# Kernel tuning notes

Hardware: AMD Instinct MI355X
Metric: run time of the kernel (lower is better)

## Reference

```python
import jax, jax.numpy as jnp
import numpy as np

REG1 = 0.5
REG2 = 0.5
ALPHA = 0.5

def setup_inputs() -> dict:
    key = jax.random.key(0)
    k1, k2, k3, k4, k5 = jax.random.split(key, 5)
    N, D, K = 32768, 256, 2048
    return {
        "encoder_out": jax.random.normal(k1, (N, D), dtype=jnp.float32),
        "prototypes": jax.random.normal(k2, (K, D), dtype=jnp.float32),
        "recon_loss": jax.random.uniform(k3, (), dtype=jnp.float32),
        "kl_loss": jax.random.uniform(k4, (), dtype=jnp.float32),
        "mmd_loss": jax.random.uniform(k5, (), dtype=jnp.float32),
    }


def _cdist_min_loss(z, prototypes):
    # torch.cdist(z, protos) -> [N, K]; f_dist = cdist(protos, z) = its transpose.
    # prototypes accessed via .data in torch -> detached.
    p = jax.lax.stop_gradient(prototypes)
    z2 = jnp.sum(z * z, axis=1, keepdims=True)          # [N, 1]
    p2 = jnp.sum(p * p, axis=1)                          # [K]
    sq = z2 + p2[None, :] - 2.0 * (z @ p.T)              # [N, K]
    dist = jnp.sqrt(jnp.maximum(sq, 0.0))
    p_min = jnp.min(dist, axis=1).mean()   # p_dist.min(1).values.mean()
    f_min = jnp.min(dist, axis=0).mean()   # f_dist [K,N].min(1) == dist.min(0)
    return REG1 * p_min + REG2 * f_min


def reference(encoder_out, prototypes, recon_loss, kl_loss, mmd_loss):
    cvae_loss = recon_loss + ALPHA * kl_loss + mmd_loss
    prot_decoding_loss = _cdist_min_loss(encoder_out, prototypes)
    # no projection head (use_projector=False)
    x = encoder_out / jnp.maximum(
        jnp.linalg.norm(encoder_out, axis=1, keepdims=True), 1e-12)
    x_mapped = x @ prototypes.T  # [N, K]
    return (encoder_out, x, x_mapped, cvae_loss, prot_decoding_loss)
```

## Files before the change

kernel.cpp:

```cpp
#include <hip/hip_runtime.h>
#include <hip/hip_bf16.h>

typedef __bf16 bf16x8 __attribute__((ext_vector_type(8)));
typedef float  f32x4  __attribute__((ext_vector_type(4)));

#define N_ROWS 32768
#define D_DIM  256
#define K_PROT 2048

#define WS_Z2    0
#define WS_INVN  32768
#define WS_P2    65536
#define WS_RMIN  67584
#define WS_CMIN  100352

#define OUT_X0   0UL
#define OUT_X1   8388608UL
#define OUT_XMAP 16777216UL
#define OUT_CVAE 83886080UL
#define OUT_PROT 83886081UL

__global__ __launch_bounds__(256) void k1_rows(
    const float* __restrict__ Z, float* __restrict__ out0, float* __restrict__ out1,
    float* __restrict__ z2, float* __restrict__ invn, unsigned int* __restrict__ rmin)
{
    int row  = (blockIdx.x << 2) + (threadIdx.x >> 6);
    int lane = threadIdx.x & 63;
    size_t base = (size_t)row * D_DIM;
    float4 v = ((const float4*)(Z + base))[lane];
    float ss = v.x*v.x + v.y*v.y + v.z*v.z + v.w*v.w;
    #pragma unroll
    for (int d = 32; d >= 1; d >>= 1) ss += __shfl_xor(ss, d);
    float inv = 1.0f / fmaxf(sqrtf(ss), 1e-12f);
    ((float4*)(out0 + base))[lane] = v;
    float4 xv; xv.x = v.x*inv; xv.y = v.y*inv; xv.z = v.z*inv; xv.w = v.w*inv;
    ((float4*)(out1 + base))[lane] = xv;
    if (lane == 0) { z2[row] = ss; invn[row] = inv; rmin[row] = 0x7f800000u; }
}

__global__ __launch_bounds__(256) void k2_prot(
    const float* __restrict__ P, float* __restrict__ p2, unsigned int* __restrict__ cmin)
{
    int row  = (blockIdx.x << 2) + (threadIdx.x >> 6);
    int lane = threadIdx.x & 63;
    float4 v = ((const float4*)(P + (size_t)row * D_DIM))[lane];
    float ss = v.x*v.x + v.y*v.y + v.z*v.z + v.w*v.w;
    #pragma unroll
    for (int d = 32; d >= 1; d >>= 1) ss += __shfl_xor(ss, d);
    if (lane == 0) { p2[row] = ss; cmin[row] = 0x7f800000u; }
}

#define BM 128
#define BN 128
#define LDSS 40

__global__ __launch_bounds__(256, 2) void k3_gemm(
    const float* __restrict__ Z, const float* __restrict__ P,
    const float* __restrict__ z2, const float* __restrict__ p2,
    const float* __restrict__ invn,
    float* __restrict__ xmap,
    unsigned int* __restrict__ rmin, unsigned int* __restrict__ cmin)
{
    __shared__ __bf16 As[BM * LDSS];
    __shared__ __bf16 Bs[BN * LDSS];

    const int tid  = threadIdx.x;
    const int bn   = blockIdx.x & 15;
    const int bm   = blockIdx.x >> 4;
    const int lane = tid & 63;
    const int wave = tid >> 6;
    const int wm   = wave >> 1;
    const int wn   = wave & 1;
    const int l15  = lane & 15;
    const int quad = lane >> 4;

    const int m0 = bm * BM;
    const int n0 = bn * BN;

    const int srow = tid >> 1;
    const int scol = (tid & 1) << 4;

    f32x4 acc[4][4];
    #pragma unroll
    for (int i = 0; i < 4; i++)
        #pragma unroll
        for (int j = 0; j < 4; j++)
            #pragma unroll
            for (int r = 0; r < 4; r++) acc[i][j][r] = 0.0f;

    for (int kt = 0; kt < D_DIM; kt += 32) {
        const float* aSrc = Z + (size_t)(m0 + srow) * D_DIM + kt + scol;
        const float* bSrc = P + (size_t)(n0 + srow) * D_DIM + kt + scol;
        float4 a0 = ((const float4*)aSrc)[0];
        float4 a1 = ((const float4*)aSrc)[1];
        float4 a2 = ((const float4*)aSrc)[2];
        float4 a3 = ((const float4*)aSrc)[3];
        float4 b0 = ((const float4*)bSrc)[0];
        float4 b1 = ((const float4*)bSrc)[1];
        float4 b2 = ((const float4*)bSrc)[2];
        float4 b3 = ((const float4*)bSrc)[3];

        __syncthreads();

        __bf16* aDst = As + srow * LDSS + scol;
        __bf16* bDst = Bs + srow * LDSS + scol;
        {
            bf16x8 w;
            w[0]=(__bf16)a0.x; w[1]=(__bf16)a0.y; w[2]=(__bf16)a0.z; w[3]=(__bf16)a0.w;
            w[4]=(__bf16)a1.x; w[5]=(__bf16)a1.y; w[6]=(__bf16)a1.z; w[7]=(__bf16)a1.w;
            *(bf16x8*)aDst = w;
            w[0]=(__bf16)a2.x; w[1]=(__bf16)a2.y; w[2]=(__bf16)a2.z; w[3]=(__bf16)a2.w;
            w[4]=(__bf16)a3.x; w[5]=(__bf16)a3.y; w[6]=(__bf16)a3.z; w[7]=(__bf16)a3.w;
            *(bf16x8*)(aDst + 8) = w;
            w[0]=(__bf16)b0.x; w[1]=(__bf16)b0.y; w[2]=(__bf16)b0.z; w[3]=(__bf16)b0.w;
            w[4]=(__bf16)b1.x; w[5]=(__bf16)b1.y; w[6]=(__bf16)b1.z; w[7]=(__bf16)b1.w;
            *(bf16x8*)bDst = w;
            w[0]=(__bf16)b2.x; w[1]=(__bf16)b2.y; w[2]=(__bf16)b2.z; w[3]=(__bf16)b2.w;
            w[4]=(__bf16)b3.x; w[5]=(__bf16)b3.y; w[6]=(__bf16)b3.z; w[7]=(__bf16)b3.w;
            *(bf16x8*)(bDst + 8) = w;
        }
        __syncthreads();

        bf16x8 af[4], bf[4];
        #pragma unroll
        for (int i = 0; i < 4; i++)
            af[i] = *(const bf16x8*)(As + (wm*64 + i*16 + l15) * LDSS + quad*8);
        #pragma unroll
        for (int j = 0; j < 4; j++)
            bf[j] = *(const bf16x8*)(Bs + (wn*64 + j*16 + l15) * LDSS + quad*8);
        #pragma unroll
        for (int i = 0; i < 4; i++)
            #pragma unroll
            for (int j = 0; j < 4; j++)
                acc[i][j] = __builtin_amdgcn_mfma_f32_16x16x32_bf16(af[i], bf[j], acc[i][j], 0, 0, 0);
    }

    float invr[16], zzr[16];
    #pragma unroll
    for (int i = 0; i < 4; i++)
        #pragma unroll
        for (int r = 0; r < 4; r++) {
            int gm = m0 + wm*64 + i*16 + quad*4 + r;
            invr[i*4+r] = invn[gm];
            zzr[i*4+r]  = z2[gm];
        }
    float pp[4];
    #pragma unroll
    for (int j = 0; j < 4; j++) pp[j] = p2[n0 + wn*64 + j*16 + l15];

    float cminv[4] = {3.0e38f, 3.0e38f, 3.0e38f, 3.0e38f};

    #pragma unroll
    for (int i = 0; i < 4; i++) {
        #pragma unroll
        for (int r = 0; r < 4; r++) {
            int gm = m0 + wm*64 + i*16 + quad*4 + r;
            float zi = zzr[i*4+r], iv = invr[i*4+r];
            size_t orow = (size_t)gm * K_PROT + n0 + wn*64 + l15;
            float rv = 3.0e38f;
            #pragma unroll
            for (int j = 0; j < 4; j++) {
                float g = acc[i][j][r];
                xmap[orow + j*16] = g * iv;
                float d = sqrtf(fmaxf(zi + pp[j] - 2.0f*g, 0.0f));
                rv = fminf(rv, d);
                cminv[j] = fminf(cminv[j], d);
            }
            #pragma unroll
            for (int s = 1; s < 16; s <<= 1) rv = fminf(rv, __shfl_xor(rv, s));
            if (l15 == 0) atomicMin(&rmin[gm], __float_as_uint(rv));
        }
    }
    #pragma unroll
    for (int j = 0; j < 4; j++) {
        float cv = cminv[j];
        cv = fminf(cv, __shfl_xor(cv, 16));
        cv = fminf(cv, __shfl_xor(cv, 32));
        if (quad == 0) atomicMin(&cmin[n0 + wn*64 + j*16 + l15], __float_as_uint(cv));
    }
}

__global__ __launch_bounds__(1024) void k4_final(
    const float* __restrict__ rminf, const float* __restrict__ cminf,
    const float* __restrict__ recon, const float* __restrict__ kl,
    const float* __restrict__ mmd, float* __restrict__ out)
{
    __shared__ float sr[16], sc[16];
    int tid = threadIdx.x;
    float a = 0.0f, b = 0.0f;
    for (int i = tid; i < N_ROWS; i += 1024) a += rminf[i];
    for (int i = tid; i < K_PROT; i += 1024) b += cminf[i];
    #pragma unroll
    for (int d = 32; d >= 1; d >>= 1) { a += __shfl_xor(a, d); b += __shfl_xor(b, d); }
    int w = tid >> 6, lane = tid & 63;
    if (lane == 0) { sr[w] = a; sc[w] = b; }
    __syncthreads();
    if (tid == 0) {
        float SA = 0.0f, SB = 0.0f;
        #pragma unroll
        for (int i = 0; i < 16; i++) { SA += sr[i]; SB += sc[i]; }
        out[OUT_CVAE] = recon[0] + 0.5f*kl[0] + mmd[0];
        out[OUT_PROT] = 0.5f*(SA / (float)N_ROWS) + 0.5f*(SB / (float)K_PROT);
    }
}

extern "C" void kernel_launch(void* const* d_in, const int* in_sizes, int n_in,
                              void* d_out, int out_size, void* d_ws, size_t ws_size,
                              hipStream_t stream)
{
    const float* Z     = (const float*)d_in[0];
    const float* P     = (const float*)d_in[1];
    const float* recon = (const float*)d_in[2];
    const float* kl    = (const float*)d_in[3];
    const float* mmd   = (const float*)d_in[4];
    float* out = (float*)d_out;
    float* ws  = (float*)d_ws;

    float* z2   = ws + WS_Z2;
    float* invn = ws + WS_INVN;
    float* p2   = ws + WS_P2;
    unsigned int* rmin = (unsigned int*)(ws + WS_RMIN);
    unsigned int* cmin = (unsigned int*)(ws + WS_CMIN);

    hipLaunchKernelGGL(k1_rows, dim3(N_ROWS/4), dim3(256), 0, stream,
                       Z, out + OUT_X0, out + OUT_X1, z2, invn, rmin);
    hipLaunchKernelGGL(k2_prot, dim3(K_PROT/4), dim3(256), 0, stream, P, p2, cmin);
    hipLaunchKernelGGL(k3_gemm, dim3((N_ROWS/BM)*(K_PROT/BN)), dim3(256), 0, stream,
                       Z, P, z2, p2, invn, out + OUT_XMAP, rmin, cmin);
    hipLaunchKernelGGL(k4_final, dim3(1), dim3(1024), 0, stream,
                       (const float*)rmin, (const float*)cmin, recon, kl, mmd, out);
}
```

Measured before the change: 443.9 us.

## Pre-convert inputs to bf16 and stage GEMM tiles via direct global-to-LDS loads

The row-norm kernels now also write bf16 copies of the encoder output and prototypes into workspace. The GEMM reads these with global_load_lds 16-byte direct-to-LDS transfers instead of loading fp32, converting in registers and storing to LDS. BK grows from 32 to 64, which halves the number of K iterations and barriers. The intent is to cut the GEMM's global traffic and VALU conversion work per tile. In exchange the unpadded LDS layout may cause bank conflicts on fragment reads, and the extra bf16 writes add traffic in the prep kernels.

```diff
diff --git a/kernel.cpp b/kernel.cpp
--- a/kernel.cpp
+++ b/kernel.cpp
@@ -2,6 +2,7 @@
 #include <hip/hip_bf16.h>
 
 typedef __bf16 bf16x8 __attribute__((ext_vector_type(8)));
+typedef __bf16 bf16x4 __attribute__((ext_vector_type(4)));
 typedef float  f32x4  __attribute__((ext_vector_type(4)));
 
 #define N_ROWS 32768
@@ -13,6 +14,8 @@
 #define WS_P2    65536
 #define WS_RMIN  67584
 #define WS_CMIN  100352
+#define WS_ZB    102400
+#define WS_PB    (102400 + 4194304)
 
 #define OUT_X0   0UL
 #define OUT_X1   8388608UL
@@ -20,9 +23,16 @@
 #define OUT_CVAE 83886080UL
 #define OUT_PROT 83886081UL
 
+__device__ __forceinline__ void gload16(const __bf16* gsrc, const __bf16* ldst) {
+    auto g = (const __attribute__((address_space(1))) unsigned int*)(unsigned long long)gsrc;
+    auto l = (__attribute__((address_space(3))) unsigned int*)(unsigned long long)ldst;
+    __builtin_amdgcn_global_load_lds(g, l, 16, 0, 0);
+}
+
 __global__ __launch_bounds__(256) void k1_rows(
     const float* __restrict__ Z, float* __restrict__ out0, float* __restrict__ out1,
-    float* __restrict__ z2, float* __restrict__ invn, unsigned int* __restrict__ rmin)
+    float* __restrict__ z2, float* __restrict__ invn, unsigned int* __restrict__ rmin,
+    __bf16* __restrict__ Zb)
 {
     int row  = (blockIdx.x << 2) + (threadIdx.x >> 6);
     int lane = threadIdx.x & 63;
@@ -35,34 +45,40 @@
     ((float4*)(out0 + base))[lane] = v;
     float4 xv; xv.x = v.x*inv; xv.y = v.y*inv; xv.z = v.z*inv; xv.w = v.w*inv;
     ((float4*)(out1 + base))[lane] = xv;
+    bf16x4 bv; bv[0]=(__bf16)v.x; bv[1]=(__bf16)v.y; bv[2]=(__bf16)v.z; bv[3]=(__bf16)v.w;
+    ((bf16x4*)(Zb + base))[lane] = bv;
     if (lane == 0) { z2[row] = ss; invn[row] = inv; rmin[row] = 0x7f800000u; }
 }
 
 __global__ __launch_bounds__(256) void k2_prot(
-    const float* __restrict__ P, float* __restrict__ p2, unsigned int* __restrict__ cmin)
+    const float* __restrict__ P, float* __restrict__ p2, unsigned int* __restrict__ cmin,
+    __bf16* __restrict__ Pb)
 {
     int row  = (blockIdx.x << 2) + (threadIdx.x >> 6);
     int lane = threadIdx.x & 63;
-    float4 v = ((const float4*)(P + (size_t)row * D_DIM))[lane];
+    size_t base = (size_t)row * D_DIM;
+    float4 v = ((const float4*)(P + base))[lane];
     float ss = v.x*v.x + v.y*v.y + v.z*v.z + v.w*v.w;
     #pragma unroll
     for (int d = 32; d >= 1; d >>= 1) ss += __shfl_xor(ss, d);
+    bf16x4 bv; bv[0]=(__bf16)v.x; bv[1]=(__bf16)v.y; bv[2]=(__bf16)v.z; bv[3]=(__bf16)v.w;
+    ((bf16x4*)(Pb + base))[lane] = bv;
     if (lane == 0) { p2[row] = ss; cmin[row] = 0x7f800000u; }
 }
 
 #define BM 128
 #define BN 128
-#define LDSS 40
+#define BK 64
 
 __global__ __launch_bounds__(256, 2) void k3_gemm(
-    const float* __restrict__ Z, const float* __restrict__ P,
+    const __bf16* __restrict__ Zb, const __bf16* __restrict__ Pb,
     const float* __restrict__ z2, const float* __restrict__ p2,
     const float* __restrict__ invn,
     float* __restrict__ xmap,
     unsigned int* __restrict__ rmin, unsigned int* __restrict__ cmin)
 {
-    __shared__ __bf16 As[BM * LDSS];
-    __shared__ __bf16 Bs[BN * LDSS];
+    __shared__ __bf16 As[BM * BK];
+    __shared__ __bf16 Bs[BN * BK];
 
     const int tid  = threadIdx.x;
     const int bn   = blockIdx.x & 15;
@@ -77,9 +93,6 @@
     const int m0 = bm * BM;
     const int n0 = bn * BN;
 
-    const int srow = tid >> 1;
-    const int scol = (tid & 1) << 4;
-
     f32x4 acc[4][4];
     #pragma unroll
     for (int i = 0; i < 4; i++)
@@ -88,51 +101,37 @@
             #pragma unroll
             for (int r = 0; r < 4; r++) acc[i][j][r] = 0.0f;
 
-    for (int kt = 0; kt < D_DIM; kt += 32) {
-        const float* aSrc = Z + (size_t)(m0 + srow) * D_DIM + kt + scol;
-        const float* bSrc = P + (size_t)(n0 + srow) * D_DIM + kt + scol;
-        float4 a0 = ((const float4*)aSrc)[0];
-        float4 a1 = ((const float4*)aSrc)[1];
-        float4 a2 = ((const float4*)aSrc)[2];
-        float4 a3 = ((const float4*)aSrc)[3];
-        float4 b0 = ((const float4*)bSrc)[0];
-        float4 b1 = ((const float4*)bSrc)[1];
-        float4 b2 = ((const float4*)bSrc)[2];
-        float4 b3 = ((const float4*)bSrc)[3];
-
+    const int ch_row[4] = {
+        ((0*4 + wave)*64 + lane) >> 3, ((1*4 + wave)*64 + lane) >> 3,
+        ((2*4 + wave)*64 + lane) >> 3, ((3*4 + wave)*64 + lane) >> 3 };
+    const int ch_c = lane & 7;
+
+    for (int kt = 0; kt < D_DIM; kt += BK) {
+        #pragma unroll
+        for (int it = 0; it < 4; it++) {
+            const __bf16* aS = Zb + (size_t)(m0 + ch_row[it]) * D_DIM + kt + ch_c * 8;
+            const __bf16* bS = Pb + (size_t)(n0 + ch_row[it]) * D_DIM + kt + ch_c * 8;
+            gload16(aS, As + (it*4 + wave) * 512);
+            gload16(bS, Bs + (it*4 + wave) * 512);
+        }
         __syncthreads();
 
-        __bf16* aDst = As + srow * LDSS + scol;
-        __bf16* bDst = Bs + srow * LDSS + scol;
-        {
-            bf16x8 w;
-            w[0]=(__bf16)a0.x; w[1]=(__bf16)a0.y; w[2]=(__bf16)a0.z; w[3]=(__bf16)a0.w;
-            w[4]=(__bf16)a1.x; w[5]=(__bf16)a1.y; w[6]=(__bf16)a1.z; w[7]=(__bf16)a1.w;
-            *(bf16x8*)aDst = w;
-            w[0]=(__bf16)a2.x; w[1]=(__bf16)a2.y; w[2]=(__bf16)a2.z; w[3]=(__bf16)a2.w;
-            w[4]=(__bf16)a3.x; w[5]=(__bf16)a3.y; w[6]=(__bf16)a3.z; w[7]=(__bf16)a3.w;
-            *(bf16x8*)(aDst + 8) = w;
-            w[0]=(__bf16)b0.x; w[1]=(__bf16)b0.y; w[2]=(__bf16)b0.z; w[3]=(__bf16)b0.w;
-            w[4]=(__bf16)b1.x; w[5]=(__bf16)b1.y; w[6]=(__bf16)b1.z; w[7]=(__bf16)b1.w;
-            *(bf16x8*)bDst = w;
-            w[0]=(__bf16)b2.x; w[1]=(__bf16)b2.y; w[2]=(__bf16)b2.z; w[3]=(__bf16)b2.w;
-            w[4]=(__bf16)b3.x; w[5]=(__bf16)b3.y; w[6]=(__bf16)b3.z; w[7]=(__bf16)b3.w;
-            *(bf16x8*)(bDst + 8) = w;
+        #pragma unroll
+        for (int s = 0; s < 2; s++) {
+            bf16x8 af[4], bfr[4];
+            #pragma unroll
+            for (int i = 0; i < 4; i++)
+                af[i] = *(const bf16x8*)(As + (wm*64 + i*16 + l15) * BK + s*32 + quad*8);
+            #pragma unroll
+            for (int j = 0; j < 4; j++)
+                bfr[j] = *(const bf16x8*)(Bs + (wn*64 + j*16 + l15) * BK + s*32 + quad*8);
+            #pragma unroll
+            for (int i = 0; i < 4; i++)
+                #pragma unroll
+                for (int j = 0; j < 4; j++)
+                    acc[i][j] = __builtin_amdgcn_mfma_f32_16x16x32_bf16(af[i], bfr[j], acc[i][j], 0, 0, 0);
         }
         __syncthreads();
-
-        bf16x8 af[4], bf[4];
-        #pragma unroll
-        for (int i = 0; i < 4; i++)
-            af[i] = *(const bf16x8*)(As + (wm*64 + i*16 + l15) * LDSS + quad*8);
-        #pragma unroll
-        for (int j = 0; j < 4; j++)
-            bf[j] = *(const bf16x8*)(Bs + (wn*64 + j*16 + l15) * LDSS + quad*8);
-        #pragma unroll
-        for (int i = 0; i < 4; i++)
-            #pragma unroll
-            for (int j = 0; j < 4; j++)
-                acc[i][j] = __builtin_amdgcn_mfma_f32_16x16x32_bf16(af[i], bf[j], acc[i][j], 0, 0, 0);
     }
 
     float invr[16], zzr[16];
@@ -221,12 +220,14 @@
     float* p2   = ws + WS_P2;
     unsigned int* rmin = (unsigned int*)(ws + WS_RMIN);
     unsigned int* cmin = (unsigned int*)(ws + WS_CMIN);
+    __bf16* Zb = (__bf16*)(ws + WS_ZB);
+    __bf16* Pb = (__bf16*)(ws + WS_PB);
 
     hipLaunchKernelGGL(k1_rows, dim3(N_ROWS/4), dim3(256), 0, stream,
-                       Z, out + OUT_X0, out + OUT_X1, z2, invn, rmin);
-    hipLaunchKernelGGL(k2_prot, dim3(K_PROT/4), dim3(256), 0, stream, P, p2, cmin);
+                       Z, out + OUT_X0, out + OUT_X1, z2, invn, rmin, Zb);
+    hipLaunchKernelGGL(k2_prot, dim3(K_PROT/4), dim3(256), 0, stream, P, p2, cmin, Pb);
     hipLaunchKernelGGL(k3_gemm, dim3((N_ROWS/BM)*(K_PROT/BN)), dim3(256), 0, stream,
-                       Z, P, z2, p2, invn, out + OUT_XMAP, rmin, cmin);
+                       Zb, Pb, z2, p2, invn, out + OUT_XMAP, rmin, cmin);
     hipLaunchKernelGGL(k4_final, dim3(1), dim3(1024), 0, stream,
                        (const float*)rmin, (const float*)cmin, recon, kl, mmd, out);
 }
```

Measured after the change: 427.8 us. 1.04x faster.
